# Performance work log

Measured on AMD Instinct MI355X. Metric: run time of the kernel, lower is better.

Reference implementation:

```python
import jax, jax.numpy as jnp
import numpy as np

N_M, N_H = 50000, 50000
E = 600000
D_IN, D_OUT = 128, 128
LN_EPS = 1e-5
NORM_EPS = 1e-12


def _segment_mean(x, seg, n):
    # PyG 'mean' aggregation: sum / count, 0 for isolated nodes (count clamped to 1)
    s = jax.ops.segment_sum(x, seg, num_segments=n)
    c = jax.ops.segment_sum(jnp.ones((seg.shape[0], 1), x.dtype), seg, num_segments=n)
    return s / jnp.maximum(c, 1.0)


def _sage(t_src, t_dst, ei, Wl, bl, Wr):
    # SAGEConv: lin_l(mean_j x_j) + lin_r(x_i), then L2-normalize rows
    agg = _segment_mean(t_src[ei[0]], ei[1], t_dst.shape[0])
    out = agg @ Wl + bl + t_dst @ Wr
    nrm = jnp.maximum(jnp.linalg.norm(out, axis=-1, keepdims=True), NORM_EPS)
    return out / nrm


def _layer_norm(x, g, b):
    mu = jnp.mean(x, axis=-1, keepdims=True)
    v = jnp.var(x, axis=-1, keepdims=True)
    return (x - mu) / jnp.sqrt(v + LN_EPS) * g + b


def setup_inputs() -> dict:
    key = jax.random.key(0)
    ks = jax.random.split(key, 24)
    r = lambda i, shape: jax.random.normal(ks[i], shape, dtype=jnp.float32) * 0.05
    inp = {
        'x_microbe': jax.random.normal(ks[0], (N_M, D_IN), dtype=jnp.float32),
        'x_host': jax.random.normal(ks[1], (N_H, D_IN), dtype=jnp.float32),
        # per-node-type linear transforms
        'W_nt_m': r(2, (D_IN, D_OUT)), 'b_nt_m': r(3, (D_OUT,)),
        'W_nt_h': r(4, (D_IN, D_OUT)), 'b_nt_h': r(5, (D_OUT,)),
        # SAGEConv params per edge type (lin_l has bias, lin_r has no bias)
        'Wl_mm': r(6, (D_OUT, D_OUT)), 'bl_mm': r(7, (D_OUT,)), 'Wr_mm': r(8, (D_OUT, D_OUT)),
        'Wl_mh': r(9, (D_OUT, D_OUT)), 'bl_mh': r(10, (D_OUT,)), 'Wr_mh': r(11, (D_OUT, D_OUT)),
        'Wl_hm': r(12, (D_OUT, D_OUT)), 'bl_hm': r(13, (D_OUT,)), 'Wr_hm': r(14, (D_OUT, D_OUT)),
        # LayerNorm affine params per node type
        'g_m': jnp.ones((D_OUT,), jnp.float32), 'be_m': jnp.zeros((D_OUT,), jnp.float32),
        'g_h': jnp.ones((D_OUT,), jnp.float32), 'be_h': jnp.zeros((D_OUT,), jnp.float32),
        # edge indices [2, E]: row0 = src, row1 = dst
        'ei_mm': jax.random.randint(ks[15], (2, E), 0, N_M, dtype=jnp.int32),
        'ei_mh': jnp.stack([jax.random.randint(ks[16], (E,), 0, N_M, dtype=jnp.int32),
                            jax.random.randint(ks[17], (E,), 0, N_H, dtype=jnp.int32)]),
        'ei_hm': jnp.stack([jax.random.randint(ks[18], (E,), 0, N_H, dtype=jnp.int32),
                            jax.random.randint(ks[19], (E,), 0, N_M, dtype=jnp.int32)]),
    }
    return inp


def reference(x_microbe, x_host, W_nt_m, b_nt_m, W_nt_h, b_nt_h,
              Wl_mm, bl_mm, Wr_mm, Wl_mh, bl_mh, Wr_mh, Wl_hm, bl_hm, Wr_hm,
              g_m, be_m, g_h, be_h, ei_mm, ei_mh, ei_hm):
    # per-type linear transforms
    t_m = x_microbe @ W_nt_m + b_nt_m
    t_h = x_host @ W_nt_h + b_nt_h
    # SAGEConv per edge type
    o_mm = _sage(t_m, t_m, ei_mm, Wl_mm, bl_mm, Wr_mm)  # microbe -> microbe
    o_mh = _sage(t_m, t_h, ei_mh, Wl_mh, bl_mh, Wr_mh)  # microbe -> host
    o_hm = _sage(t_h, t_m, ei_hm, Wl_hm, bl_hm, Wr_hm)  # host -> microbe
    # HeteroConv aggr='mean' over edge types per dst node type
    conv_m = 0.5 * (o_mm + o_hm)
    conv_h = o_mh
    # residual + LayerNorm (dropout is identity in eval mode)
    out_m = _layer_norm(t_m + conv_m, g_m, be_m)
    out_h = _layer_norm(t_h + conv_h, g_h, be_h)
    return out_m, out_h
```

## Files before the change

### kernel.cpp

```cpp
#include <hip/hip_runtime.h>

typedef unsigned short u16;
typedef unsigned int u32;
typedef __attribute__((ext_vector_type(8))) short bf16x8;
typedef __attribute__((ext_vector_type(4))) float f32x4;

#define LDSN 13312
#define CHUNK 16384

__device__ __forceinline__ float bf_lo(u32 u){ return __uint_as_float(u << 16); }
__device__ __forceinline__ float bf_hi(u32 u){ return __uint_as_float(u & 0xffff0000u); }
__device__ __forceinline__ float bf2f(u16 v){ return __uint_as_float((u32)v << 16); }
__device__ __forceinline__ u16 f2bf(float f){
    u32 u = __float_as_uint(f);
    u32 r = (u + 0x7fffu + ((u >> 16) & 1u)) >> 16;
    return (u16)r;
}
__device__ __forceinline__ u32 pack2(float a, float b){
    return (u32)f2bf(a) | ((u32)f2bf(b) << 16);
}

__global__ __launch_bounds__(256) void fusedA_kernel(
    const int* __restrict__ d0, const int* __restrict__ d1, const int* __restrict__ d2,
    u16* __restrict__ rk0, u16* __restrict__ rk1, u16* __restrict__ rk2,
    int E0, int E1, int E2, int n0, int n1, int n2,
    int c0, int c1, int c2, int R0, int R1, int R2,
    u16* __restrict__ C0, u16* __restrict__ C1, u16* __restrict__ C2, int HB2,
    const float* __restrict__ Wf0, const float* __restrict__ Wf1,
    const float* __restrict__ Wf2, const float* __restrict__ Wf3,
    const float* __restrict__ Wf4, const float* __restrict__ Wf5,
    u16* __restrict__ WF,
    const float* __restrict__ Xm, const float* __restrict__ Wm,
    const float* __restrict__ bm, u16* __restrict__ Tm, int NM,
    const float* __restrict__ Xh, const float* __restrict__ Wh,
    const float* __restrict__ bh, u16* __restrict__ Th, int NH,
    int gm, int gh)
{
    __shared__ u32 lc[LDSN / 2];
    int bid = blockIdx.x;
    if (bid < HB2){
        const int* dp; u16 *rk, *cp; int E, n, cc, rr;
        if (bid < c0 * R0){ dp = d0; rk = rk0; cp = C0; E = E0; n = n0; cc = bid / R0; rr = bid % R0; }
        else if (bid < c0 * R0 + c1 * R1){ int l = bid - c0 * R0; dp = d1; rk = rk1; cp = C1; E = E1; n = n1; cc = l / R1; rr = l % R1; }
        else { int l = bid - c0 * R0 - c1 * R1; dp = d2; rk = rk2; cp = C2; E = E2; n = n2; cc = l / R2; rr = l % R2; }
        for (int i = threadIdx.x; i < LDSN / 2; i += 256) lc[i] = 0;
        __syncthreads();
        int r0 = rr * LDSN, r1 = min(r0 + LDSN, n);
        int i0 = cc * CHUNK, i1 = min(i0 + CHUNK, E);
        for (int i = i0 + threadIdx.x; i < i1; i += 256){
            int x = dp[i];
            if ((unsigned)x < (unsigned)n && x >= r0 && x < r1){
                int lx = x - r0;
                int sh = (lx & 1) << 4;
                u32 old = atomicAdd(&lc[lx >> 1], 1u << sh);
                rk[i] = (u16)((old >> sh) & 0xffffu);
            }
        }
        __syncthreads();
        u16* op = cp + (size_t)cc * n;
        for (int x = r0 + threadIdx.x; x < r1; x += 256){
            int lx = x - r0;
            op[x] = (u16)((lc[lx >> 1] >> ((lx & 1) << 4)) & 0xffffu);
        }
        return;
    }
    bid -= HB2;
    if (bid < 6){
        const float* W = bid == 0 ? Wf0 : bid == 1 ? Wf1 : bid == 2 ? Wf2 :
                         bid == 3 ? Wf3 : bid == 4 ? Wf4 : Wf5;
        u16* dst = WF + (size_t)bid * 16384;
        #pragma unroll 4
        for (int k = 0; k < 64; ++k){
            int i = k * 256 + threadIdx.x;
            int j   = i & 7;
            int l16 = (i >> 3) & 15;
            int qd  = (i >> 7) & 3;
            int q   = (i >> 9) & 3;
            int tt  = (i >> 11) & 1;
            int w   = (i >> 12) & 3;
            dst[i] = f2bf(W[(q * 32 + qd * 8 + j) * 128 + (w * 32 + tt * 16 + l16)]);
        }
        return;
    }
    bid -= 6;
    const float *A, *W, *bias; u16* C; int N, lgrid, lbid;
    if (bid < gm){ A = Xm; W = Wm; bias = bm; C = Tm; N = NM; lgrid = gm; lbid = bid; }
    else         { A = Xh; W = Wh; bias = bh; C = Th; N = NH; lgrid = gh; lbid = bid - gm; }

    int tid = threadIdx.x;
    int wave = tid >> 6, lane = tid & 63;
    int colHalf = wave & 1;
    int ln16 = lane & 15, quad = lane >> 4;

    bf16x8 Bfrag[4][4];
    #pragma unroll
    for (int t = 0; t < 4; ++t){
        int col = colHalf * 64 + t * 16 + ln16;
        #pragma unroll
        for (int q = 0; q < 4; ++q){
            bf16x8 f;
            #pragma unroll
            for (int j = 0; j < 8; ++j)
                f[j] = (short)f2bf(W[(q * 32 + quad * 8 + j) * 128 + col]);
            Bfrag[t][q] = f;
        }
    }
    float bv[4];
    #pragma unroll
    for (int t = 0; t < 4; ++t)
        bv[t] = bias[colHalf * 64 + t * 16 + ln16];

    int rowBlocks = (N + 15) >> 4;
    for (int rb = lbid * 2 + (wave >> 1); rb < rowBlocks; rb += lgrid * 2){
        int row0 = rb * 16;
        int ar = row0 + ln16; if (ar > N - 1) ar = N - 1;
        const float* Arow = A + (size_t)ar * 128 + quad * 8;
        bf16x8 Af[4];
        #pragma unroll
        for (int q = 0; q < 4; ++q){
            f32x4 lo = *(const f32x4*)(Arow + q * 32);
            f32x4 hi = *(const f32x4*)(Arow + q * 32 + 4);
            bf16x8 f;
            #pragma unroll
            for (int j = 0; j < 4; ++j){ f[j] = (short)f2bf(lo[j]); f[4+j] = (short)f2bf(hi[j]); }
            Af[q] = f;
        }
        f32x4 acc[4];
        #pragma unroll
        for (int t = 0; t < 4; ++t) acc[t] = (f32x4){bv[t], bv[t], bv[t], bv[t]};
        #pragma unroll
        for (int q = 0; q < 4; ++q)
            #pragma unroll
            for (int t = 0; t < 4; ++t)
                acc[t] = __builtin_amdgcn_mfma_f32_16x16x32_bf16(Af[q], Bfrag[t][q], acc[t], 0, 0, 0);
        #pragma unroll
        for (int t = 0; t < 4; ++t){
            int col = colHalf * 64 + t * 16 + ln16;
            #pragma unroll
            for (int r = 0; r < 4; ++r){
                int row = row0 + quad * 4 + r;
                if (row < N) C[(size_t)row * 128 + col] = f2bf(acc[t][r]);
            }
        }
    }
}

__global__ __launch_bounds__(256) void scan_blocks_kernel(
    const u16* __restrict__ C0, const u16* __restrict__ C1, const u16* __restrict__ C2,
    int c0, int c1, int c2, int NM, int NH, int n,
    int* __restrict__ off, int* __restrict__ part)
{
    __shared__ int lds[256];
    int tid = threadIdx.x;
    int base = blockIdx.x * 2048 + tid * 8;
    int v[8]; int s = 0;
    #pragma unroll
    for (int j = 0; j < 8; ++j){
        int idx = base + j;
        int tot = 0;
        if (idx < n){
            const u16* cp; int ch, w, x;
            if (idx < NM){ cp = C0; ch = c0; w = NM; x = idx; }
            else if (idx < 2 * NM){ cp = C1; ch = c1; w = NM; x = idx - NM; }
            else { cp = C2; ch = c2; w = NH; x = idx - 2 * NM; }
            for (int cc = 0; cc < ch; ++cc) tot += cp[(size_t)cc * w + x];
        }
        v[j] = s; s += tot;
    }
    lds[tid] = s;
    __syncthreads();
    for (int d = 1; d < 256; d <<= 1){
        int t = (tid >= d) ? lds[tid - d] : 0;
        __syncthreads();
        lds[tid] += t;
        __syncthreads();
    }
    int thrBase = (tid > 0) ? lds[tid - 1] : 0;
    if (tid == 255) part[blockIdx.x] = lds[255];
    #pragma unroll
    for (int j = 0; j < 8; ++j){
        int idx = base + j;
        if (idx < n) off[idx] = thrBase + v[j];
    }
}

__global__ __launch_bounds__(128) void scan_part_kernel(
    int* __restrict__ part, int np, int* __restrict__ total_slot)
{
    __shared__ int lds[128];
    int tid = threadIdx.x;
    lds[tid] = (tid < np) ? part[tid] : 0;
    __syncthreads();
    for (int d = 1; d < 128; d <<= 1){
        int t = (tid >= d) ? lds[tid - d] : 0;
        __syncthreads();
        lds[tid] += t;
        __syncthreads();
    }
    if (tid < np) part[tid] = (tid > 0) ? lds[tid - 1] : 0;
    if (tid == 0) *total_slot = lds[np - 1 < 0 ? 0 : np - 1];
}

__global__ __launch_bounds__(256) void colbase_kernel(
    const u16* __restrict__ C0, const u16* __restrict__ C1, const u16* __restrict__ C2,
    int* __restrict__ B0, int* __restrict__ B1, int* __restrict__ B2,
    int c0, int c1, int c2, int NM, int NH, int n,
    int* __restrict__ off, const int* __restrict__ part)
{
    int idx = blockIdx.x * 256 + threadIdx.x;
    if (idx >= n) return;
    int run = off[idx] + part[idx >> 11];
    off[idx] = run;
    const u16* cp; int* bp; int ch, w, x;
    if (idx < NM){ cp = C0; bp = B0; ch = c0; w = NM; x = idx; }
    else if (idx < 2 * NM){ cp = C1; bp = B1; ch = c1; w = NM; x = idx - NM; }
    else { cp = C2; bp = B2; ch = c2; w = NH; x = idx - 2 * NM; }
    for (int cc = 0; cc < ch; ++cc){
        bp[(size_t)cc * w + x] = run;
        run += cp[(size_t)cc * w + x];
    }
}

__global__ __launch_bounds__(256) void fill3_kernel(
    const int* __restrict__ s0, const int* __restrict__ s1, const int* __restrict__ s2,
    const int* __restrict__ d0, const int* __restrict__ d1, const int* __restrict__ d2,
    const u16* __restrict__ rk0, const u16* __restrict__ rk1, const u16* __restrict__ rk2,
    int E0, int E1, int E2, int n0, int n1, int n2,
    const int* __restrict__ B0, const int* __restrict__ B1, const int* __restrict__ B2,
    int* __restrict__ slot)
{
    int t = blockIdx.y;
    const int* sp = t == 0 ? s0 : (t == 1 ? s1 : s2);
    const int* dp = t == 0 ? d0 : (t == 1 ? d1 : d2);
    const u16* rk = t == 0 ? rk0 : (t == 1 ? rk1 : rk2);
    const int* bp = t == 0 ? B0 : (t == 1 ? B1 : B2);
    int E = t == 0 ? E0 : (t == 1 ? E1 : E2);
    int n = t == 0 ? n0 : (t == 1 ? n1 : n2);
    int base = blockIdx.x * 1024 + threadIdx.x;
    #pragma unroll
    for (int k = 0; k < 4; ++k){
        int i = base + k * 256;
        if (i < E){
            int x = dp[i];
            if ((unsigned)x < (unsigned)n){
                int cc = i / CHUNK;
                slot[bp[(size_t)cc * n + x] + (int)rk[i]] = sp[i];
            }
        }
    }
}

__global__ __launch_bounds__(256) void gather3_kernel(
    const u16* __restrict__ TM, const u16* __restrict__ TH,
    const int* __restrict__ off, const int* __restrict__ slot,
    u32* __restrict__ AGGM, u32* __restrict__ AGGH, int NM, int NH)
{
    int n3 = 2 * NM + NH;
    int wid = (int)((blockIdx.x * 256u + threadIdx.x) >> 6);
    int lane = threadIdx.x & 63;
    int nw = (gridDim.x * 256) >> 6;

    for (int id0 = wid * 4; id0 < n3; id0 += nw * 4){
        int bb[4], dg[4], tk[4], ms[4], ns[4];
        const u16* Ts[4];
        #pragma unroll
        for (int r = 0; r < 4; ++r){
            int id = id0 + r;
            int b = 0, e = 0;
            if (id < n3){ b = off[id]; e = off[id + 1]; }
            bb[r] = b;
            int deg = e - b; dg[r] = deg;
            int take = deg < 64 ? deg : 64; tk[r] = take;
            const u16* Tsrc; int nsrc;
            if (id < NM){ Tsrc = TM; nsrc = NM; }
            else if (id < 2 * NM){ Tsrc = TH; nsrc = NH; }
            else { Tsrc = TM; nsrc = NM; }
            Ts[r] = Tsrc; ns[r] = nsrc;
            int s = 0;
            if (lane < take){
                s = slot[b + lane];
                if ((unsigned)s >= (unsigned)nsrc) s = 0;
            }
            ms[r] = s;
        }

        #pragma unroll
        for (int r = 0; r < 4; ++r){
            int id = id0 + r;
            if (id >= n3) break;
            const u16* Tsrc = Ts[r];
            int take = tk[r];
            float a0=0.f,a1=0.f,b0f=0.f,b1f=0.f,c0=0.f,c1=0.f,d0f=0.f,d1f=0.f;
            float e0=0.f,e1=0.f,f0=0.f,f1=0.f,g0=0.f,g1=0.f,h0=0.f,h1=0.f;
            int j = 0;
            for (; j + 8 <= take; j += 8){
                int i0 = __shfl(ms[r], j);     int i1 = __shfl(ms[r], j + 1);
                int i2 = __shfl(ms[r], j + 2); int i3 = __shfl(ms[r], j + 3);
                int i4 = __shfl(ms[r], j + 4); int i5 = __shfl(ms[r], j + 5);
                int i6 = __shfl(ms[r], j + 6); int i7 = __shfl(ms[r], j + 7);
                u32 u0 = *(const u32*)(Tsrc + (size_t)i0 * 128 + lane * 2);
                u32 u1 = *(const u32*)(Tsrc + (size_t)i1 * 128 + lane * 2);
                u32 u2 = *(const u32*)(Tsrc + (size_t)i2 * 128 + lane * 2);
                u32 u3 = *(const u32*)(Tsrc + (size_t)i3 * 128 + lane * 2);
                u32 u4 = *(const u32*)(Tsrc + (size_t)i4 * 128 + lane * 2);
                u32 u5 = *(const u32*)(Tsrc + (size_t)i5 * 128 + lane * 2);
                u32 u6 = *(const u32*)(Tsrc + (size_t)i6 * 128 + lane * 2);
                u32 u7 = *(const u32*)(Tsrc + (size_t)i7 * 128 + lane * 2);
                a0 += bf_lo(u0); a1 += bf_hi(u0);
                b0f += bf_lo(u1); b1f += bf_hi(u1);
                c0 += bf_lo(u2); c1 += bf_hi(u2);
                d0f += bf_lo(u3); d1f += bf_hi(u3);
                e0 += bf_lo(u4); e1 += bf_hi(u4);
                f0 += bf_lo(u5); f1 += bf_hi(u5);
                g0 += bf_lo(u6); g1 += bf_hi(u6);
                h0 += bf_lo(u7); h1 += bf_hi(u7);
            }
            for (; j + 4 <= take; j += 4){
                int i0 = __shfl(ms[r], j);     int i1 = __shfl(ms[r], j + 1);
                int i2 = __shfl(ms[r], j + 2); int i3 = __shfl(ms[r], j + 3);
                u32 u0 = *(const u32*)(Tsrc + (size_t)i0 * 128 + lane * 2);
                u32 u1 = *(const u32*)(Tsrc + (size_t)i1 * 128 + lane * 2);
                u32 u2 = *(const u32*)(Tsrc + (size_t)i2 * 128 + lane * 2);
                u32 u3 = *(const u32*)(Tsrc + (size_t)i3 * 128 + lane * 2);
                a0 += bf_lo(u0); a1 += bf_hi(u0);
                b0f += bf_lo(u1); b1f += bf_hi(u1);
                c0 += bf_lo(u2); c1 += bf_hi(u2);
                d0f += bf_lo(u3); d1f += bf_hi(u3);
            }
            for (; j < take; ++j){
                int i0 = __shfl(ms[r], j);
                u32 u0 = *(const u32*)(Tsrc + (size_t)i0 * 128 + lane * 2);
                a0 += bf_lo(u0); a1 += bf_hi(u0);
            }
            for (int j2 = bb[r] + 64; j2 < bb[r] + dg[r]; ++j2){
                int i0 = slot[j2];
                if ((unsigned)i0 >= (unsigned)ns[r]) i0 = 0;
                u32 u0 = *(const u32*)(Tsrc + (size_t)i0 * 128 + lane * 2);
                a0 += bf_lo(u0); a1 += bf_hi(u0);
            }
            float s0 = ((a0 + b0f) + (c0 + d0f)) + ((e0 + f0) + (g0 + h0));
            float s1 = ((a1 + b1f) + (c1 + d1f)) + ((e1 + f1) + (g1 + h1));
            float inv = 1.0f / (float)(dg[r] < 1 ? 1 : dg[r]);
            u32 pv = pack2(s0 * inv, s1 * inv);
            if (id < 2 * NM) AGGM[(size_t)id * 64 + lane] = pv;
            else             AGGH[(size_t)(id - 2 * NM) * 64 + lane] = pv;
        }
    }
}

template<int NT>
__global__ __launch_bounds__(256) void gemmln_kernel(
    const u32* __restrict__ AG1, const u32* __restrict__ AG2,
    const u16* __restrict__ Tdst,
    const u16* __restrict__ WFl1, const u16* __restrict__ WFr1, const float* __restrict__ bl1,
    const u16* __restrict__ WFl2, const u16* __restrict__ WFr2, const float* __restrict__ bl2,
    const float* __restrict__ g, const float* __restrict__ be,
    float* __restrict__ outp, int N, float scale)
{
    __shared__ float redN[NT][4][16];
    __shared__ float redS[2][4][16];

    int tid = threadIdx.x;
    int wave = tid >> 6, lane = tid & 63;
    int ln16 = lane & 15, quad = lane >> 4;

    const u32* AG[2] = {AG1, AG2};
    const u16* WFl[2] = {WFl1, WFl2};
    const u16* WFr[2] = {WFr1, WFr2};
    const float* bls[2] = {bl1, bl2};

    bf16x8 BL[NT][2][4], BR[NT][2][4];
    float bv[NT][2];
    #pragma unroll
    for (int et = 0; et < NT; ++et){
        #pragma unroll
        for (int t = 0; t < 2; ++t){
            bv[et][t] = bls[et][wave * 32 + t * 16 + ln16];
            #pragma unroll
            for (int q = 0; q < 4; ++q){
                int fo = ((((wave * 2 + t) * 4 + q) * 4 + quad) * 16 + ln16) * 8;
                BL[et][t][q] = *(const bf16x8*)(WFl[et] + fo);
                BR[et][t][q] = *(const bf16x8*)(WFr[et] + fo);
            }
        }
    }
    float gv[2], bev[2];
    #pragma unroll
    for (int t = 0; t < 2; ++t){
        int col = wave * 32 + t * 16 + ln16;
        gv[t] = g[col]; bev[t] = be[col];
    }

    int tiles = (N + 15) >> 4;
    for (int tile = blockIdx.x; tile < tiles; tile += gridDim.x){
        int row0 = tile * 16;
        int ar = row0 + ln16; if (ar > N - 1) ar = N - 1;
        const u16* Ar2 = Tdst + (size_t)ar * 128 + quad * 8;

        f32x4 acc[NT][2];
        #pragma unroll
        for (int et = 0; et < NT; ++et)
            #pragma unroll
            for (int t = 0; t < 2; ++t)
                acc[et][t] = (f32x4){bv[et][t], bv[et][t], bv[et][t], bv[et][t]};

        #pragma unroll
        for (int q = 0; q < 4; ++q){
            bf16x8 afr = *(const bf16x8*)(Ar2 + q * 32);
            #pragma unroll
            for (int et = 0; et < NT; ++et){
                bf16x8 afl = *(const bf16x8*)(AG[et] + (size_t)ar * 64 + q * 16 + quad * 4);
                #pragma unroll
                for (int t = 0; t < 2; ++t){
                    acc[et][t] = __builtin_amdgcn_mfma_f32_16x16x32_bf16(afl, BL[et][t][q], acc[et][t], 0, 0, 0);
                    acc[et][t] = __builtin_amdgcn_mfma_f32_16x16x32_bf16(afr, BR[et][t][q], acc[et][t], 0, 0, 0);
                }
            }
        }

        #pragma unroll
        for (int et = 0; et < NT; ++et){
            #pragma unroll
            for (int r = 0; r < 4; ++r){
                float s = acc[et][0][r] * acc[et][0][r] + acc[et][1][r] * acc[et][1][r];
                #pragma unroll
                for (int m = 1; m < 16; m <<= 1) s += __shfl_xor(s, m);
                if (ln16 == 0) redN[et][wave][quad * 4 + r] = s;
            }
        }
        __syncthreads();

        float yv[2][4];
        float lsum[4], lsq[4];
        #pragma unroll
        for (int r = 0; r < 4; ++r){
            int r16 = quad * 4 + r;
            int row = row0 + r16;
            int crow = row < N ? row : N - 1;
            float sc[NT];
            #pragma unroll
            for (int et = 0; et < NT; ++et){
                float tot = redN[et][0][r16] + redN[et][1][r16] + redN[et][2][r16] + redN[et][3][r16];
                sc[et] = scale / fmaxf(sqrtf(tot), 1e-12f);
            }
            float s1v = 0.f, s2v = 0.f;
            #pragma unroll
            for (int t = 0; t < 2; ++t){
                int col = wave * 32 + t * 16 + ln16;
                float y = bf2f(Tdst[(size_t)crow * 128 + col]);
                #pragma unroll
                for (int et = 0; et < NT; ++et) y += acc[et][t][r] * sc[et];
                yv[t][r] = y;
                s1v += y; s2v += y * y;
            }
            #pragma unroll
            for (int m = 1; m < 16; m <<= 1){ s1v += __shfl_xor(s1v, m); s2v += __shfl_xor(s2v, m); }
            lsum[r] = s1v; lsq[r] = s2v;
        }
        if (ln16 == 0){
            #pragma unroll
            for (int r = 0; r < 4; ++r){
                redS[0][wave][quad * 4 + r] = lsum[r];
                redS[1][wave][quad * 4 + r] = lsq[r];
            }
        }
        __syncthreads();

        #pragma unroll
        for (int r = 0; r < 4; ++r){
            int r16 = quad * 4 + r;
            int row = row0 + r16;
            if (row >= N) continue;
            float S1 = redS[0][0][r16] + redS[0][1][r16] + redS[0][2][r16] + redS[0][3][r16];
            float S2 = redS[1][0][r16] + redS[1][1][r16] + redS[1][2][r16] + redS[1][3][r16];
            float mean = S1 * (1.0f / 128.0f);
            float var = S2 * (1.0f / 128.0f) - mean * mean;
            float rstd = rsqrtf(var + 1e-5f);
            #pragma unroll
            for (int t = 0; t < 2; ++t){
                int col = wave * 32 + t * 16 + ln16;
                outp[(size_t)row * 128 + col] = (yv[t][r] - mean) * rstd * gv[t] + bev[t];
            }
        }
        __syncthreads();
    }
}

extern "C" void kernel_launch(void* const* d_in, const int* in_sizes, int n_in,
                              void* d_out, int out_size, void* d_ws, size_t ws_size,
                              hipStream_t stream) {
    const float* xm    = (const float*)d_in[0];
    const float* xh    = (const float*)d_in[1];
    const float* Wnt_m = (const float*)d_in[2];  const float* bnt_m = (const float*)d_in[3];
    const float* Wnt_h = (const float*)d_in[4];  const float* bnt_h = (const float*)d_in[5];
    const float* Wl_mm = (const float*)d_in[6];  const float* bl_mm = (const float*)d_in[7];
    const float* Wr_mm = (const float*)d_in[8];
    const float* Wl_mh = (const float*)d_in[9];  const float* bl_mh = (const float*)d_in[10];
    const float* Wr_mh = (const float*)d_in[11];
    const float* Wl_hm = (const float*)d_in[12]; const float* bl_hm = (const float*)d_in[13];
    const float* Wr_hm = (const float*)d_in[14];
    const float* g_m   = (const float*)d_in[15]; const float* be_m  = (const float*)d_in[16];
    const float* g_h   = (const float*)d_in[17]; const float* be_h  = (const float*)d_in[18];
    const int* ei_mm = (const int*)d_in[19];
    const int* ei_mh = (const int*)d_in[20];
    const int* ei_hm = (const int*)d_in[21];

    const int D = 128;
    const int NM = in_sizes[0] / D;
    const int NH = in_sizes[1] / D;
    const int E1 = in_sizes[19] / 2;
    const int E2 = in_sizes[20] / 2;
    const int E3 = in_sizes[21] / 2;
    const int Esum = E1 + E2 + E3;
    const int n3 = 2 * NM + NH;

    const int c0 = (E1 + CHUNK - 1) / CHUNK;
    const int c1 = (E3 + CHUNK - 1) / CHUNK;
    const int c2 = (E2 + CHUNK - 1) / CHUNK;
    const int R0 = (NM + LDSN - 1) / LDSN;
    const int R1 = (NM + LDSN - 1) / LDSN;
    const int R2 = (NH + LDSN - 1) / LDSN;
    const int HB2 = c0 * R0 + c1 * R1 + c2 * R2;

    char* ws = (char*)d_ws;
    size_t woff = 0;
    auto alloc = [&](size_t bytes) -> void* {
        void* p = ws + woff;
        woff += (bytes + 255) & ~(size_t)255;
        return p;
    };
    u16* T_M   = (u16*)alloc((size_t)NM * D * 2);
    u16* T_H   = (u16*)alloc((size_t)NH * D * 2);
    u16* CNT16 = (u16*)alloc(((size_t)(c0 + c1) * NM + (size_t)c2 * NH) * 2);
    int* OFF3  = (int*)alloc((size_t)(n3 + 1) * 4);
    int* SLOT3 = (int*)alloc((size_t)Esum * 4);
    int* PART  = (int*)alloc(1024 * 4);
    u16* WF    = (u16*)alloc((size_t)6 * 16384 * 2);
    u32* AGGM  = (u32*)alloc((size_t)2 * NM * 64 * 4);
    if (woff > ws_size) return;

    u16* C0p = CNT16;
    u16* C1p = C0p + (size_t)c0 * NM;
    u16* C2p = C1p + (size_t)c1 * NM;

    int* B0p = (int*)d_out;
    int* B1p = B0p + (size_t)c0 * NM;
    int* B2p = B1p + (size_t)c1 * NM;
    u16* RK  = (u16*)(B2p + (size_t)c2 * NH);
    u16* rk0 = RK, *rk1 = RK + E1, *rk2 = RK + E1 + E3;
    u32* AGGH = (u32*)d_out;

    float* OUT_M = (float*)d_out;
    float* OUT_H = (float*)d_out + (size_t)NM * D;

    const int gm = 1024, gh = 1024;
    const int scanBlocks = (n3 + 2047) / 2048;
    int Emax = E1 > E2 ? E1 : E2; if (E3 > Emax) Emax = E3;
    const dim3 egrid((Emax + 1023) / 1024, 3);

    fusedA_kernel<<<HB2 + 6 + gm + gh, 256, 0, stream>>>(
        ei_mm + E1, ei_hm + E3, ei_mh + E2,
        rk0, rk1, rk2,
        E1, E3, E2, NM, NM, NH,
        c0, c1, c2, R0, R1, R2,
        C0p, C1p, C2p, HB2,
        Wl_mm, Wr_mm, Wl_hm, Wr_hm, Wl_mh, Wr_mh, WF,
        xm, Wnt_m, bnt_m, T_M, NM,
        xh, Wnt_h, bnt_h, T_H, NH, gm, gh);

    scan_blocks_kernel<<<scanBlocks, 256, 0, stream>>>(
        C0p, C1p, C2p, c0, c1, c2, NM, NH, n3, OFF3, PART);
    scan_part_kernel<<<1, 128, 0, stream>>>(PART, scanBlocks, OFF3 + n3);
    colbase_kernel<<<(n3 + 255) / 256, 256, 0, stream>>>(
        C0p, C1p, C2p, B0p, B1p, B2p, c0, c1, c2, NM, NH, n3, OFF3, PART);

    fill3_kernel<<<egrid, 256, 0, stream>>>(
        ei_mm, ei_hm, ei_mh,
        ei_mm + E1, ei_hm + E3, ei_mh + E2,
        rk0, rk1, rk2,
        E1, E3, E2, NM, NM, NH,
        B0p, B1p, B2p, SLOT3);

    gather3_kernel<<<2048, 256, 0, stream>>>(
        T_M, T_H, OFF3, SLOT3, AGGM, AGGH, NM, NH);

    gemmln_kernel<1><<<1024, 256, 0, stream>>>(
        AGGH, nullptr, T_H,
        WF + 4 * 16384, WF + 5 * 16384, bl_mh,
        nullptr, nullptr, nullptr,
        g_h, be_h, OUT_H, NH, 1.0f);
    gemmln_kernel<2><<<1024, 256, 0, stream>>>(
        AGGM, AGGM + (size_t)NM * 64, T_M,
        WF + 0 * 16384, WF + 1 * 16384, bl_mm,
        WF + 2 * 16384, WF + 3 * 16384, bl_hm,
        g_m, be_m, OUT_M, NM, 0.5f);
}
```

Before: 455.5 us.

## Enlarge count chunk, unroll histogram loop, fold partial scan into colbase, widen gather grid

The edge chunk per counting block grows from 16K to 128K, so fewer chunk columns need to be scanned, and the counting loop is unrolled four-way to issue independent index loads together. The separate single-block scan over partial sums is removed; each colbase thread instead sums the preceding partials serially and the last thread writes the total. The gather kernel grid is doubled. Larger chunks reduce the number of count blocks, which lowers parallelism in the histogram phase but shrinks the per-column base arrays and the colbase loop length.

```diff
diff --git a/kernel.cpp b/kernel.cpp
--- a/kernel.cpp
+++ b/kernel.cpp
@@ -6,7 +6,7 @@
 typedef __attribute__((ext_vector_type(4))) float f32x4;
 
 #define LDSN 13312
-#define CHUNK 16384
+#define CHUNK 131072
 
 __device__ __forceinline__ float bf_lo(u32 u){ return __uint_as_float(u << 16); }
 __device__ __forceinline__ float bf_hi(u32 u){ return __uint_as_float(u & 0xffff0000u); }
@@ -47,7 +47,31 @@
         __syncthreads();
         int r0 = rr * LDSN, r1 = min(r0 + LDSN, n);
         int i0 = cc * CHUNK, i1 = min(i0 + CHUNK, E);
-        for (int i = i0 + threadIdx.x; i < i1; i += 256){
+        int i = i0 + threadIdx.x;
+        for (; i + 768 < i1; i += 1024){
+            int xa = dp[i], xb = dp[i + 256], xc = dp[i + 512], xd = dp[i + 768];
+            if ((unsigned)xa < (unsigned)n && xa >= r0 && xa < r1){
+                int lx = xa - r0; int sh = (lx & 1) << 4;
+                u32 old = atomicAdd(&lc[lx >> 1], 1u << sh);
+                rk[i] = (u16)((old >> sh) & 0xffffu);
+            }
+            if ((unsigned)xb < (unsigned)n && xb >= r0 && xb < r1){
+                int lx = xb - r0; int sh = (lx & 1) << 4;
+                u32 old = atomicAdd(&lc[lx >> 1], 1u << sh);
+                rk[i + 256] = (u16)((old >> sh) & 0xffffu);
+            }
+            if ((unsigned)xc < (unsigned)n && xc >= r0 && xc < r1){
+                int lx = xc - r0; int sh = (lx & 1) << 4;
+                u32 old = atomicAdd(&lc[lx >> 1], 1u << sh);
+                rk[i + 512] = (u16)((old >> sh) & 0xffffu);
+            }
+            if ((unsigned)xd < (unsigned)n && xd >= r0 && xd < r1){
+                int lx = xd - r0; int sh = (lx & 1) << 4;
+                u32 old = atomicAdd(&lc[lx >> 1], 1u << sh);
+                rk[i + 768] = (u16)((old >> sh) & 0xffffu);
+            }
+        }
+        for (; i < i1; i += 256){
             int x = dp[i];
             if ((unsigned)x < (unsigned)n && x >= r0 && x < r1){
                 int lx = x - r0;
@@ -184,23 +208,6 @@
     }
 }
 
-__global__ __launch_bounds__(128) void scan_part_kernel(
-    int* __restrict__ part, int np, int* __restrict__ total_slot)
-{
-    __shared__ int lds[128];
-    int tid = threadIdx.x;
-    lds[tid] = (tid < np) ? part[tid] : 0;
-    __syncthreads();
-    for (int d = 1; d < 128; d <<= 1){
-        int t = (tid >= d) ? lds[tid - d] : 0;
-        __syncthreads();
-        lds[tid] += t;
-        __syncthreads();
-    }
-    if (tid < np) part[tid] = (tid > 0) ? lds[tid - 1] : 0;
-    if (tid == 0) *total_slot = lds[np - 1 < 0 ? 0 : np - 1];
-}
-
 __global__ __launch_bounds__(256) void colbase_kernel(
     const u16* __restrict__ C0, const u16* __restrict__ C1, const u16* __restrict__ C2,
     int* __restrict__ B0, int* __restrict__ B1, int* __restrict__ B2,
@@ -209,7 +216,10 @@
 {
     int idx = blockIdx.x * 256 + threadIdx.x;
     if (idx >= n) return;
-    int run = off[idx] + part[idx >> 11];
+    int pb = idx >> 11;
+    int p = 0;
+    for (int k = 0; k < pb; ++k) p += part[k];
+    int run = off[idx] + p;
     off[idx] = run;
     const u16* cp; int* bp; int ch, w, x;
     if (idx < NM){ cp = C0; bp = B0; ch = c0; w = NM; x = idx; }
@@ -219,6 +229,7 @@
         bp[(size_t)cc * w + x] = run;
         run += cp[(size_t)cc * w + x];
     }
+    if (idx == n - 1) off[n] = run;
 }
 
 __global__ __launch_bounds__(256) void fill3_kernel(
@@ -570,7 +581,6 @@
 
     scan_blocks_kernel<<<scanBlocks, 256, 0, stream>>>(
         C0p, C1p, C2p, c0, c1, c2, NM, NH, n3, OFF3, PART);
-    scan_part_kernel<<<1, 128, 0, stream>>>(PART, scanBlocks, OFF3 + n3);
     colbase_kernel<<<(n3 + 255) / 256, 256, 0, stream>>>(
         C0p, C1p, C2p, B0p, B1p, B2p, c0, c1, c2, NM, NH, n3, OFF3, PART);
 
@@ -581,7 +591,7 @@
         E1, E3, E2, NM, NM, NH,
         B0p, B1p, B2p, SLOT3);
 
-    gather3_kernel<<<2048, 256, 0, stream>>>(
+    gather3_kernel<<<4096, 256, 0, stream>>>(
         T_M, T_H, OFF3, SLOT3, AGGM, AGGH, NM, NH);
 
     gemmln_kernel<1><<<1024, 256, 0, stream>>>(
```

Result: slower. 480.7 us (+5.5%).
